# Kernel optimization log

Hardware: AMD Instinct MI355X
Metric: run time of the kernel (lower is better)

## Reference

```python
import jax, jax.numpy as jnp
import numpy as np

WIN = 7
K1, K2 = 0.01, 0.03


def _box_filter(x, w):
    """Valid-padding uniform box filter. x: (B, D, H, W); w: (1, 1, k, k)."""
    B, D, H, Wd = x.shape
    k = w.shape[-1]
    y = jax.lax.conv_general_dilated(
        x.reshape(B * D, 1, H, Wd), w, window_strides=(1, 1), padding='VALID',
        dimension_numbers=('NCHW', 'OIHW', 'NCHW'))
    return y.reshape(B, D, H - k + 1, Wd - k + 1)


def setup_inputs() -> dict:
    key = jax.random.key(0)
    kx, ky = jax.random.split(key)
    X = jax.random.uniform(kx, (4, 64, 256, 256), dtype=jnp.float32)
    Y = jax.random.uniform(ky, (4, 64, 256, 256), dtype=jnp.float32)
    w = jnp.ones((1, 1, WIN, WIN), dtype=jnp.float32) / (WIN * WIN)  # buffer self.w
    return {"X": X, "Y": Y, "w": w}


def reference(X, Y, w):
    data_range = 1.0
    C1 = (K1 * data_range) ** 2
    C2 = (K2 * data_range) ** 2
    NP = WIN * WIN
    cov_norm = NP / (NP - 1)

    ux = _box_filter(X, w)
    uy = _box_filter(Y, w)
    uxx = _box_filter(X * X, w)
    uyy = _box_filter(Y * Y, w)
    uxy = _box_filter(X * Y, w)

    vx = cov_norm * (uxx - ux * ux)
    vy = cov_norm * (uyy - uy * uy)
    vxy = cov_norm * (uxy - ux * uy)

    A1 = 2.0 * ux * uy + C1
    A2 = 2.0 * vxy + C2
    B1 = ux * ux + uy * uy + C1
    B2 = vx + vy + C2
    S = (A1 * A2) / (B1 * B2)  # (B, D, H', W')

    # Faithful to torch: ssim_per_slice[:, i] = S_i.mean() (mean over batch AND spatial),
    # then 1 - mean over depth, returned per batch element.
    slice_means = S.mean(axis=(0, 2, 3))  # (D,)
    loss = 1.0 - slice_means.mean()
    return jnp.full((X.shape[0],), loss, dtype=X.dtype)
```

## Files before the change

kernel.cpp:

```cpp
#include <hip/hip_runtime.h>

#define H 256
#define W 256
#define W4 (W / 4)
#define OWID 250
#define OHEI 250
#define NIMG 256
#define BAND 28
#define NBANDS 9
#define NBLK (NBANDS * NIMG)
#define VPAD 264

__device__ __forceinline__ float4 f4zero() { return make_float4(0.f, 0.f, 0.f, 0.f); }

__device__ __forceinline__ void vacc(float4& s, const float4 n, const float4 o) {
    s.x += n.x - o.x; s.y += n.y - o.y; s.z += n.z - o.z; s.w += n.w - o.w;
}
__device__ __forceinline__ void vaccp(float4& s, const float4 a, const float4 b,
                                      const float4 c, const float4 d) {
    s.x += a.x * b.x - c.x * d.x;
    s.y += a.y * b.y - c.y * d.y;
    s.z += a.z * b.z - c.z * d.z;
    s.w += a.w * b.w - c.w * d.w;
}

__global__ __launch_bounds__(64) void ssim_band_kernel(
    const float* __restrict__ X, const float* __restrict__ Y,
    float* __restrict__ partial)
{
    __shared__ float vsx[VPAD], vsy[VPAD], vsxx[VPAD], vsyy[VPAD], vsxy[VPAD];

    const int lane = threadIdx.x;
    const int band = blockIdx.x;
    const int img  = blockIdx.y;
    const int r0 = band * BAND;
    const int out_rows = (OHEI - r0 < BAND) ? (OHEI - r0) : BAND;
    const int rows_in = out_rows + 6;

    const float4* Xp = (const float4*)X + ((size_t)img * H + r0) * W4 + lane;
    const float4* Yp = (const float4*)Y + ((size_t)img * H + r0) * W4 + lane;

    float4 xh[7], yh[7];
    float4 sx = f4zero(), sy = f4zero(), sxx = f4zero(), syy = f4zero(), sxy = f4zero();

    #pragma unroll
    for (int i = 0; i < 6; ++i) {
        float4 xv = Xp[i * W4];
        float4 yv = Yp[i * W4];
        xh[i] = xv; yh[i] = yv;
        vacc(sx, xv, f4zero());
        vacc(sy, yv, f4zero());
        vaccp(sxx, xv, xv, f4zero(), f4zero());
        vaccp(syy, yv, yv, f4zero(), f4zero());
        vaccp(sxy, xv, yv, f4zero(), f4zero());
    }
    xh[6] = f4zero(); yh[6] = f4zero();

    float4 xn = Xp[6 * W4];
    float4 yn = Yp[6 * W4];

    const float inv_np   = 1.0f / 49.0f;
    const float cov_norm = 49.0f / 48.0f;
    const float C1 = 1e-4f;
    const float C2 = 9e-4f;
    float lsum = 0.0f;

    for (int base = 6; base < rows_in; base += 7) {
        #pragma unroll
        for (int i = 0; i < 7; ++i) {
            const int r = base + i;
            if (r < rows_in) {
                const int slot = (6 + i) % 7;
                float4 xf, yf;
                const bool more = (r + 1 < rows_in);
                if (more) { xf = Xp[(r + 1) * W4]; yf = Yp[(r + 1) * W4]; }

                const float4 xo = xh[slot], yo = yh[slot];
                vacc(sx, xn, xo);
                vacc(sy, yn, yo);
                vaccp(sxx, xn, xn, xo, xo);
                vaccp(syy, yn, yn, yo, yo);
                vaccp(sxy, xn, yn, xo, yo);
                xh[slot] = xn; yh[slot] = yn;

                ((float4*)vsx)[lane] = sx;
                ((float4*)vsy)[lane] = sy;
                ((float4*)vsxx)[lane] = sxx;
                ((float4*)vsyy)[lane] = syy;
                ((float4*)vsxy)[lane] = sxy;
                __syncthreads();

                float wx[4], wy[4], wxx[4], wyy[4], wxy[4];
                #define HWIN(VS, S, WA)                                        \
                {                                                              \
                    float4 b = ((const float4*)VS)[lane + 1];                  \
                    float2 c = *(const float2*)&VS[4 * lane + 8];              \
                    WA[0] = S.x + S.y + S.z + S.w + b.x + b.y + b.z;           \
                    WA[1] = WA[0] - S.x + b.w;                                 \
                    WA[2] = WA[1] - S.y + c.x;                                 \
                    WA[3] = WA[2] - S.z + c.y;                                 \
                }
                HWIN(vsx,  sx,  wx)
                HWIN(vsy,  sy,  wy)
                HWIN(vsxx, sxx, wxx)
                HWIN(vsyy, syy, wyy)
                HWIN(vsxy, sxy, wxy)
                #undef HWIN
                __syncthreads();

                #pragma unroll
                for (int s = 0; s < 4; ++s) {
                    float ux  = wx[s]  * inv_np;
                    float uy  = wy[s]  * inv_np;
                    float uxx = wxx[s] * inv_np;
                    float uyy = wyy[s] * inv_np;
                    float uxy = wxy[s] * inv_np;
                    float vx  = cov_norm * (uxx - ux * ux);
                    float vy  = cov_norm * (uyy - uy * uy);
                    float vxy = cov_norm * (uxy - ux * uy);
                    float A1 = 2.f * ux * uy + C1;
                    float A2 = 2.f * vxy + C2;
                    float B1 = ux * ux + uy * uy + C1;
                    float B2 = vx + vy + C2;
                    float S = (A1 * A2) * __builtin_amdgcn_rcpf(B1 * B2);
                    if (4 * lane + s < OWID) lsum += S;
                }
                xn = xf; yn = yf;
            }
        }
    }

    #pragma unroll
    for (int off = 32; off > 0; off >>= 1)
        lsum += __shfl_down(lsum, off, 64);
    if (lane == 0) partial[img * NBANDS + band] = lsum;
}

__global__ __launch_bounds__(256) void ssim_reduce_kernel(
    const float* __restrict__ partial, float* __restrict__ out)
{
    const int tid = threadIdx.x;
    double acc = 0.0;
    for (int i = tid; i < NBLK; i += 256)
        acc += (double)partial[i];
    #pragma unroll
    for (int off = 32; off > 0; off >>= 1)
        acc += __shfl_down(acc, off, 64);
    __shared__ double wsumd[4];
    if ((tid & 63) == 0) wsumd[tid >> 6] = acc;
    __syncthreads();
    if (tid == 0) {
        double total = wsumd[0] + wsumd[1] + wsumd[2] + wsumd[3];
        float loss = (float)(1.0 - total / 16000000.0);
        out[0] = loss; out[1] = loss; out[2] = loss; out[3] = loss;
    }
}

extern "C" void kernel_launch(void* const* d_in, const int* in_sizes, int n_in,
                              void* d_out, int out_size, void* d_ws, size_t ws_size,
                              hipStream_t stream) {
    const float* X = (const float*)d_in[0];
    const float* Y = (const float*)d_in[1];
    float* out = (float*)d_out;
    float* partial = (float*)d_ws;

    hipLaunchKernelGGL(ssim_band_kernel, dim3(NBANDS, NIMG), dim3(64), 0, stream,
                       X, Y, partial);
    hipLaunchKernelGGL(ssim_reduce_kernel, dim3(1), dim3(256), 0, stream,
                       partial, out);
}
```

Measured before the change: 161.1 us.

## Replace LDS horizontal window with wave shuffles, fold SSIM constants, halve band height

```diff
diff --git a/kernel.cpp b/kernel.cpp
--- a/kernel.cpp
+++ b/kernel.cpp
@@ -6,10 +6,9 @@
 #define OWID 250
 #define OHEI 250
 #define NIMG 256
-#define BAND 28
-#define NBANDS 9
+#define BAND 14
+#define NBANDS 18
 #define NBLK (NBANDS * NIMG)
-#define VPAD 264
 
 __device__ __forceinline__ float4 f4zero() { return make_float4(0.f, 0.f, 0.f, 0.f); }
 
@@ -28,8 +27,6 @@
     const float* __restrict__ X, const float* __restrict__ Y,
     float* __restrict__ partial)
 {
-    __shared__ float vsx[VPAD], vsy[VPAD], vsxx[VPAD], vsyy[VPAD], vsxy[VPAD];
-
     const int lane = threadIdx.x;
     const int band = blockIdx.x;
     const int img  = blockIdx.y;
@@ -59,10 +56,14 @@
     float4 xn = Xp[6 * W4];
     float4 yn = Yp[6 * W4];
 
-    const float inv_np   = 1.0f / 49.0f;
-    const float cov_norm = 49.0f / 48.0f;
-    const float C1 = 1e-4f;
-    const float C2 = 9e-4f;
+    const float C1  = 1e-4f;
+    const float C2  = 9e-4f;
+    const float AA  = 1.f / 2401.f;
+    const float C2A = 2.f / 2401.f;
+    const float T1  = 1.f / 24.f;
+    const float T2  = -1.f / 1176.f;
+    const float T3  = 1.f / 48.f;
+    const float T4  = -1.f / 2352.f;
     float lsum = 0.0f;
 
     for (int base = 6; base < rows_in; base += 7) {
@@ -83,46 +84,37 @@
                 vaccp(sxy, xn, yn, xo, yo);
                 xh[slot] = xn; yh[slot] = yn;
 
-                ((float4*)vsx)[lane] = sx;
-                ((float4*)vsy)[lane] = sy;
-                ((float4*)vsxx)[lane] = sxx;
-                ((float4*)vsyy)[lane] = syy;
-                ((float4*)vsxy)[lane] = sxy;
-                __syncthreads();
-
                 float wx[4], wy[4], wxx[4], wyy[4], wxy[4];
-                #define HWIN(VS, S, WA)                                        \
+                #define HWIN(S, WA)                                            \
                 {                                                              \
-                    float4 b = ((const float4*)VS)[lane + 1];                  \
-                    float2 c = *(const float2*)&VS[4 * lane + 8];              \
-                    WA[0] = S.x + S.y + S.z + S.w + b.x + b.y + b.z;           \
-                    WA[1] = WA[0] - S.x + b.w;                                 \
-                    WA[2] = WA[1] - S.y + c.x;                                 \
-                    WA[3] = WA[2] - S.z + c.y;                                 \
+                    const float bx = __shfl_down(S.x, 1);                      \
+                    const float by = __shfl_down(S.y, 1);                      \
+                    const float bz = __shfl_down(S.z, 1);                      \
+                    const float bw = __shfl_down(S.w, 1);                      \
+                    const float cx = __shfl_down(S.x, 2);                      \
+                    const float cy = __shfl_down(S.y, 2);                      \
+                    WA[0] = S.x + S.y + S.z + S.w + bx + by + bz;              \
+                    WA[1] = WA[0] - S.x + bw;                                  \
+                    WA[2] = WA[1] - S.y + cx;                                  \
+                    WA[3] = WA[2] - S.z + cy;                                  \
                 }
-                HWIN(vsx,  sx,  wx)
-                HWIN(vsy,  sy,  wy)
-                HWIN(vsxx, sxx, wxx)
-                HWIN(vsyy, syy, wyy)
-                HWIN(vsxy, sxy, wxy)
+                HWIN(sx,  wx)
+                HWIN(sy,  wy)
+                HWIN(sxx, wxx)
+                HWIN(syy, wyy)
+                HWIN(sxy, wxy)
                 #undef HWIN
-                __syncthreads();
 
                 #pragma unroll
                 for (int s = 0; s < 4; ++s) {
-                    float ux  = wx[s]  * inv_np;
-                    float uy  = wy[s]  * inv_np;
-                    float uxx = wxx[s] * inv_np;
-                    float uyy = wyy[s] * inv_np;
-                    float uxy = wxy[s] * inv_np;
-                    float vx  = cov_norm * (uxx - ux * ux);
-                    float vy  = cov_norm * (uyy - uy * uy);
-                    float vxy = cov_norm * (uxy - ux * uy);
-                    float A1 = 2.f * ux * uy + C1;
-                    float A2 = 2.f * vxy + C2;
-                    float B1 = ux * ux + uy * uy + C1;
-                    float B2 = vx + vy + C2;
-                    float S = (A1 * A2) * __builtin_amdgcn_rcpf(B1 * B2);
+                    const float P  = wx[s] * wy[s];
+                    const float Qs = fmaf(wy[s], wy[s], wx[s] * wx[s]);
+                    const float Ws = wxx[s] + wyy[s];
+                    const float A1 = fmaf(C2A, P, C1);
+                    const float B1 = fmaf(AA, Qs, C1);
+                    const float A2 = fmaf(T1, wxy[s], fmaf(T2, P, C2));
+                    const float B2 = fmaf(T3, Ws, fmaf(T4, Qs, C2));
+                    const float S  = (A1 * A2) * __builtin_amdgcn_rcpf(B1 * B2);
                     if (4 * lane + s < OWID) lsum += S;
                 }
                 xn = xf; yn = yf;
```

Result: no change. 161.3 us (+0.1%).
